# Kernel optimization log

Measured on AMD Instinct MI355X. Metric: run time of the kernel, lower is better.

Reference implementation:

```python
import jax, jax.numpy as jnp
import numpy as np

# Skeleton structure (start, end) connections
REAL_CONNECTIONS = [(0,1),(1,2),(2,3),(3,4),(1,5),(5,6),(6,7),(7,8),(8,9),(8,13),(8,17),(8,21),(8,25),(9,10),(10,11),(11,12),(13,14),(14,15),(15,16),(17,18),(18,19),(19,20),(21,22),(22,23),(23,24),(25,26),(26,27),(27,28),(4,29),(29,30),(29,34),(29,38),(29,42),(29,46),(30,31),(31,32),(32,33),(34,35),(35,36),(36,37),(38,39),(39,40),(40,41),(42,43),(43,44),(44,45),(46,47),(47,48),(48,49)]

def _bone_ranges():
    # dict insertion order matters only for iteration; result is a sum so order-free
    ranges = {(0,1):(0.05,0.15),(1,2):(0.1,0.2),(1,5):(0.1,0.2),(2,3):(0.2,0.35),(3,4):(0.2,0.35),(5,6):(0.2,0.35),(6,7):(0.2,0.35),(4,8):(0.05,0.15),(7,29):(0.05,0.15)}
    for s, e in REAL_CONNECTIONS:
        if 8 <= s < 50 and 8 <= e < 50:
            ranges[(s, e)] = (0.01, 0.08)
    return ranges

_BR = _bone_ranges()
BONE_S = np.array([k[0] for k in _BR], np.int32)
BONE_E = np.array([k[1] for k in _BR], np.int32)
BONE_MIN = np.array([v[0] for v in _BR.values()], np.float32)
BONE_MAX = np.array([v[1] for v in _BR.values()], np.float32)

SYM_L = np.array([8 + i for i in range(21)] + [2, 3, 4], np.int32)
SYM_R = np.array([29 + i for i in range(21)] + [5, 6, 7], np.int32)

ANG_A = np.array([1, 1, 2, 5], np.int32)
ANG_B = np.array([2, 5, 3, 6], np.int32)
ANG_C = np.array([3, 6, 4, 7], np.int32)

CONN_S = np.array([c[0] for c in REAL_CONNECTIONS], np.int32)
CONN_E = np.array([c[1] for c in REAL_CONNECTIONS], np.int32)

DEG = np.float32(180.0 / np.pi)
EPS = np.float32(1e-12)

def _relu(x):
    return jnp.maximum(x, 0.0)

def _normalize(v):
    n = jnp.linalg.norm(v, axis=-1, keepdims=True)
    return v / jnp.maximum(n, EPS)

def setup_inputs() -> dict:
    key = jax.random.key(0)
    k1, k2 = jax.random.split(key)
    B, S, D = 64, 2048, 150
    pred_poses = jax.random.normal(k1, (B, S, D), dtype=jnp.float32)
    target_poses = jax.random.normal(k2, (B, S, D), dtype=jnp.float32)
    return {"pred_poses": pred_poses, "target_poses": target_poses}

def reference(pred_poses, target_poses):
    B, S, _ = pred_poses.shape
    J = pred_poses.reshape(B, S, 50, 3)
    T = target_poses.reshape(B, S, 50, 3)

    # ---- bone length loss (49 constrained bones, one gathered pass) ----
    bv = J[:, :, BONE_E] - J[:, :, BONE_S]                 # [B,S,49,3]
    bl = jnp.linalg.norm(bv, axis=-1)                      # [B,S,49]
    bone_pen = _relu(bl - BONE_MAX) + _relu(BONE_MIN - bl)
    bone_loss = bone_pen.mean()  # == sum over bones of per-bone mean / n_bones

    # ---- joint angle loss (4 triples) ----
    v1 = _normalize(J[:, :, ANG_A] - J[:, :, ANG_B])       # [B,S,4,3]
    v2 = _normalize(J[:, :, ANG_C] - J[:, :, ANG_B])
    cos = jnp.clip(jnp.sum(v1 * v2, axis=-1), -1.0, 1.0)
    deg = jnp.arccos(cos) * DEG
    angle_loss = (_relu(30.0 - deg) + _relu(deg - 150.0)).mean()

    # ---- symmetry loss (24 pairs) ----
    L = J[:, :, SYM_L]                                     # [B,S,24,3]
    R = J[:, :, SYM_R]
    x_sym = jnp.abs(L[..., 0] + R[..., 0])                 # [B,S,24]
    yz_sim = jnp.abs(L[..., 1:] - R[..., 1:]).mean(axis=-1)
    symmetry_loss = (x_sym + yz_sim).mean()

    # ---- temporal consistency ----
    vel = J[:, 1:] - J[:, :-1]                             # [B,S-1,50,3]
    acc = vel[:, 1:] - vel[:, :-1]
    temporal_loss = jnp.linalg.norm(acc, axis=-1).mean() + 0.5 * jnp.linalg.norm(vel, axis=-1).mean()

    # ---- supervised bone-length consistency (all 49 connections) ----
    tb = jnp.linalg.norm(T[:, :, CONN_E] - T[:, :, CONN_S], axis=-1)
    pb = jnp.linalg.norm(J[:, :, CONN_E] - J[:, :, CONN_S], axis=-1)
    supervised_loss = jnp.abs(pb - tb).mean()

    total = (1.0 * bone_loss + 0.5 * angle_loss + 0.3 * symmetry_loss
             + 0.2 * temporal_loss + supervised_loss)
    return bone_loss, angle_loss, symmetry_loss, temporal_loss, supervised_loss, total
```

## Files before the change

kernel.cpp:

```cpp
#include <hip/hip_runtime.h>
#include <math.h>

#define TPB 512
#define CH  32
#define CPB 8

static constexpr int B_     = 64;
static constexpr int S_     = 2048;
static constexpr int TOTAL  = B_ * S_;
static constexpr int NCHUNK = TOTAL / CH;
static constexpr int NBLK   = NCHUNK / CPB;
static constexpr int SAMPB  = 600;
static constexpr int PREDB  = (CH + 2) * SAMPB;
static constexpr int TGTB   = CH * SAMPB;
static constexpr int CHB    = PREDB + TGTB;
static constexpr int NSLICE = 39;
static constexpr int BUFB   = NSLICE * 1024;
static constexpr long TOTB  = (long)TOTAL * SAMPB;

__constant__ int US_[51] = {0,1,1,2,3,5,6,4,7,7,4,
    8,8,8,8,8,9,10,11,13,14,
    15,17,18,19,21,22,23,25,26,27,
    29,29,29,29,29,30,31,32,34,35,
    36,38,39,40,42,43,44,46,47,48};
__constant__ int UE_[51] = {1,2,5,3,4,6,7,8,29,8,29,
    9,13,17,21,25,10,11,12,14,15,
    16,18,19,20,22,23,24,26,27,28,
    30,34,38,42,46,31,32,33,35,36,
    37,39,40,41,43,44,45,47,48,49};
__constant__ float UMIN11_[11] = {0.05f,0.1f,0.1f,0.2f,0.2f,0.2f,0.2f,0.05f,0.05f,-1e9f,-1e9f};
__constant__ float UMAX11_[11] = {0.15f,0.2f,0.2f,0.35f,0.35f,0.35f,0.35f,0.15f,0.15f,1e9f,1e9f};
__constant__ float WSUP11_[11] = {1.f,1.f,1.f,1.f,1.f,1.f,1.f,0.f,0.f,1.f,1.f};
__constant__ int SL_[24] = {8,9,10,11,12,13,14,15,16,17,18,19,20,21,22,23,24,25,26,27,28,2,3,4};
__constant__ int SR_[24] = {29,30,31,32,33,34,35,36,37,38,39,40,41,42,43,44,45,46,47,48,49,5,6,7};
__constant__ int AJ_[4] = {1,1,2,5};
__constant__ int BJ_[4] = {2,5,3,6};
__constant__ int CJ_[4] = {3,6,4,7};

struct F3 { float x, y, z; };
__device__ __forceinline__ F3 ld3(const float* p) { return *(const F3*)p; }
#define SQRTF __builtin_amdgcn_sqrtf

typedef const __attribute__((address_space(1))) void* gas_t;
typedef __attribute__((address_space(3))) void* las_t;

__global__ __launch_bounds__(TPB, 4) void pose_main(
    const float* __restrict__ pred, const float* __restrict__ tgt,
    float* __restrict__ part)
{
    __shared__ __align__(16) char LDS[2 * BUFB];

    const int tid = threadIdx.x;
    const int blk = blockIdx.x;
    const int li  = tid & 15;
    const int g   = tid >> 4;

    const int   uOs0 = US_[g] * 3, uOe0 = UE_[g] * 3;
    const float uMn0 = (g < 11) ? UMIN11_[g] : 0.01f;
    const float uMx0 = (g < 11) ? UMAX11_[g] : 0.08f;
    const float uW0  = (g < 11) ? WSUP11_[g] : 1.f;
    const bool  u1_on = (g < 19);
    const int   k1   = u1_on ? g + 32 : 50;
    const int   uOs1 = US_[k1] * 3, uOe1 = UE_[k1] * 3;
    const bool sy_on = (g < 24);
    const int  ksy = sy_on ? g : 0;
    const int  syL = SL_[ksy] * 3, syR = SR_[ksy] * 3;
    const int aAo = AJ_[g & 3] * 3, aBo = BJ_[g & 3] * 3, aCo = CJ_[g & 3] * 3;
    const int  tO0 = g * 3;
    const int  tO1 = (g + 32) * 3;
    const bool t1_on = (g < 18);

    float a_bone = 0.f, a_ang = 0.f, a_sym = 0.f, a_vel = 0.f, a_acc = 0.f, a_sup = 0.f;

    const int w      = tid >> 6;
    const int lane16 = (tid & 63) << 4;
    auto stage = [&](int cidx, char* lbuf) {
        const long nb = (long)cidx * TGTB;
        const char* pb = (const char*)pred + nb;
        const char* tb = (const char*)tgt  + nb - PREDB;
        const long prem = TOTB - nb - 16;
        #pragma unroll
        for (int s = 0; s < 5; ++s) {
            const int slice = w + s * 8;
            if (slice < NSLICE) {
                const long o = (long)slice * 1024 + lane16;
                const char* src = (o < PREDB)
                    ? pb + (o > prem ? prem : o)
                    : tb + (o > (long)(CHB - 16) ? (long)(CHB - 16) : o);
                __builtin_amdgcn_global_load_lds((gas_t)src, (las_t)(lbuf + slice * 1024), 16, 0, 0);
            }
        }
    };

    const int c0 = blk * CPB;
    stage(c0, LDS);

    #pragma unroll
    for (int c = 0; c < CPB; ++c) {
        char* curb = LDS + (c & 1) * BUFB;
        char* nxtb = LDS + ((c & 1) ^ 1) * BUFB;
        if (c + 1 < CPB) {
            stage(c0 + c + 1, nxtb);
            if (w < 7) asm volatile("s_waitcnt vmcnt(5)" ::: "memory");
            else       asm volatile("s_waitcnt vmcnt(4)" ::: "memory");
        } else {
            asm volatile("s_waitcnt vmcnt(0)" ::: "memory");
        }
        __builtin_amdgcn_s_barrier();
        __builtin_amdgcn_sched_barrier(0);

        const float* Jl = (const float*)curb;
        const float* Tl = Jl + PREDB / 4;
        const int s_base = ((c0 + c) * CH) & (S_ - 1);

        #pragma unroll
        for (int h = 0; h < 2; ++h) {
            const int sb = (li + h * 16) * 150;
            const float* Jp = Jl + sb;
            const float* Tp = Tl + sb;

            auto edge = [&](int so, int eo, float mn, float mx, float wsup) {
                const F3 je = ld3(Jp + eo), js = ld3(Jp + so);
                const float dx = je.x - js.x, dy = je.y - js.y, dz = je.z - js.z;
                const float pb = SQRTF(dx * dx + dy * dy + dz * dz);
                a_bone += fmaxf(pb - mx, 0.f) + fmaxf(mn - pb, 0.f);
                const F3 te = ld3(Tp + eo), ts = ld3(Tp + so);
                const float tx = te.x - ts.x, ty = te.y - ts.y, tz = te.z - ts.z;
                const float tb = SQRTF(tx * tx + ty * ty + tz * tz);
                a_sup += wsup * fabsf(pb - tb);
            };
            edge(uOs0, uOe0, uMn0, uMx0, uW0);
            if (u1_on) edge(uOs1, uOe1, 0.01f, 0.08f, 1.f);

            if (sy_on) {
                const F3 L = ld3(Jp + syL), R = ld3(Jp + syR);
                a_sym += fabsf(L.x + R.x) + 0.5f * (fabsf(L.y - R.y) + fabsf(L.z - R.z));
            }

            if (g < 4) {
                const F3 A = ld3(Jp + aAo), Bb = ld3(Jp + aBo), C = ld3(Jp + aCo);
                const float v1x = A.x - Bb.x, v1y = A.y - Bb.y, v1z = A.z - Bb.z;
                const float v2x = C.x - Bb.x, v2y = C.y - Bb.y, v2z = C.z - Bb.z;
                const float n12 = (v1x*v1x + v1y*v1y + v1z*v1z) * (v2x*v2x + v2y*v2y + v2z*v2z);
                const float inv = __frsqrt_rn(fmaxf(n12, 1e-24f));
                float cosv = (v1x*v2x + v1y*v2y + v1z*v2z) * inv;
                cosv = fminf(fmaxf(cosv, -1.f), 1.f);
                const float deg = acosf(cosv) * 57.29577951308232f;
                a_ang += fmaxf(30.f - deg, 0.f) + fmaxf(deg - 150.f, 0.f);
            }

            {
                const int sidx = s_base + li + h * 16;
                const bool v_ok = sidx < S_ - 1;
                const bool a_ok = sidx < S_ - 2;
                auto temporal = [&](int off) {
                    const F3 p0 = ld3(Jp + off), p1 = ld3(Jp + off + 150), p2 = ld3(Jp + off + 300);
                    if (v_ok) {
                        const float vx = p1.x - p0.x, vy = p1.y - p0.y, vz = p1.z - p0.z;
                        a_vel += SQRTF(vx*vx + vy*vy + vz*vz);
                        if (a_ok) {
                            const float ax = p2.x - 2.f*p1.x + p0.x;
                            const float ay = p2.y - 2.f*p1.y + p0.y;
                            const float az = p2.z - 2.f*p1.z + p0.z;
                            a_acc += SQRTF(ax*ax + ay*ay + az*az);
                        }
                    }
                };
                temporal(tO0);
                if (t1_on) temporal(tO1);
            }
        }

        asm volatile("" ::: "memory");
        __builtin_amdgcn_s_barrier();
    }

    float vals[6] = {a_bone, a_ang, a_sym, a_vel, a_acc, a_sup};
    #pragma unroll
    for (int k = 0; k < 6; ++k)
        #pragma unroll
        for (int off = 32; off > 0; off >>= 1)
            vals[k] += __shfl_down(vals[k], off, 64);

    float* red = (float*)LDS;
    const int lane = tid & 63;
    if (lane == 0) {
        #pragma unroll
        for (int k = 0; k < 6; ++k) red[w * 6 + k] = vals[k];
    }
    __syncthreads();
    if (tid == 0) {
        #pragma unroll
        for (int k = 0; k < 6; ++k) {
            float s = 0.f;
            #pragma unroll
            for (int v = 0; v < 8; ++v) s += red[v * 6 + k];
            part[k * NBLK + blk] = s;
        }
    }
}

__global__ __launch_bounds__(256) void pose_reduce(
    const float* __restrict__ part, float* __restrict__ out)
{
    __shared__ float red[4][6];
    const int tid = threadIdx.x;
    float a[6];
    #pragma unroll
    for (int k = 0; k < 6; ++k) {
        float s = 0.f;
        for (int i = tid; i < NBLK; i += 256) s += part[k * NBLK + i];
        a[k] = s;
    }
    #pragma unroll
    for (int k = 0; k < 6; ++k)
        #pragma unroll
        for (int off = 32; off > 0; off >>= 1)
            a[k] += __shfl_down(a[k], off, 64);

    const int wid = tid >> 6, lane = tid & 63;
    if (lane == 0) {
        #pragma unroll
        for (int k = 0; k < 6; ++k) red[wid][k] = a[k];
    }
    __syncthreads();
    if (tid == 0) {
        float t[6];
        #pragma unroll
        for (int k = 0; k < 6; ++k) t[k] = red[0][k] + red[1][k] + red[2][k] + red[3][k];
        const float bone = t[0] * (1.f / ((float)TOTAL * 49.f));
        const float ang  = t[1] * (1.f / ((float)TOTAL * 4.f));
        const float sym  = t[2] * (1.f / ((float)TOTAL * 24.f));
        const float temporal = t[4] * (1.f / ((float)B_ * (float)(S_ - 2) * 50.f))
                             + 0.5f * t[3] * (1.f / ((float)B_ * (float)(S_ - 1) * 50.f));
        const float sup  = t[5] * (1.f / ((float)TOTAL * 49.f));
        out[0] = bone;
        out[1] = ang;
        out[2] = sym;
        out[3] = temporal;
        out[4] = sup;
        out[5] = bone + 0.5f * ang + 0.3f * sym + 0.2f * temporal + sup;
    }
}

extern "C" void kernel_launch(void* const* d_in, const int* in_sizes, int n_in,
                              void* d_out, int out_size, void* d_ws, size_t ws_size,
                              hipStream_t stream)
{
    const float* pred = (const float*)d_in[0];
    const float* tgt  = (const float*)d_in[1];
    float* part = (float*)d_ws;
    pose_main<<<NBLK, TPB, 0, stream>>>(pred, tgt, part);
    pose_reduce<<<1, 256, 0, stream>>>(part, (float*)d_out);
}
```

Before: 39.64 us.

## Fuse final reduction into main kernel and regroup bone and temporal work

```diff
diff --git a/kernel.cpp b/kernel.cpp
--- a/kernel.cpp
+++ b/kernel.cpp
@@ -18,19 +18,9 @@
 static constexpr int BUFB   = NSLICE * 1024;
 static constexpr long TOTB  = (long)TOTAL * SAMPB;
 
-__constant__ int US_[51] = {0,1,1,2,3,5,6,4,7,7,4,
-    8,8,8,8,8,9,10,11,13,14,
-    15,17,18,19,21,22,23,25,26,27,
-    29,29,29,29,29,30,31,32,34,35,
-    36,38,39,40,42,43,44,46,47,48};
-__constant__ int UE_[51] = {1,2,5,3,4,6,7,8,29,8,29,
-    9,13,17,21,25,10,11,12,14,15,
-    16,18,19,20,22,23,24,26,27,28,
-    30,34,38,42,46,31,32,33,35,36,
-    37,39,40,41,43,44,45,47,48,49};
-__constant__ float UMIN11_[11] = {0.05f,0.1f,0.1f,0.2f,0.2f,0.2f,0.2f,0.05f,0.05f,-1e9f,-1e9f};
-__constant__ float UMAX11_[11] = {0.15f,0.2f,0.2f,0.35f,0.35f,0.35f,0.35f,0.15f,0.15f,1e9f,1e9f};
-__constant__ float WSUP11_[11] = {1.f,1.f,1.f,1.f,1.f,1.f,1.f,0.f,0.f,1.f,1.f};
+__constant__ int CA_[26] = {0,2,1,6,7,  8,10,8,14,8,18,8,22,8,26,  29,31,29,35,29,39,29,43,29,47, 4};
+__constant__ int CB_[26] = {1,3,5,7,29, 9,11,13,15,17,19,21,23,25,27, 30,32,34,36,38,40,42,44,46,48, 8};
+__constant__ int CC_[26] = {2,4,6,8,4,  10,12,14,16,18,20,22,24,26,28, 31,33,35,37,39,41,43,45,47,49, 8};
 __constant__ int SL_[24] = {8,9,10,11,12,13,14,15,16,17,18,19,20,21,22,23,24,25,26,27,28,2,3,4};
 __constant__ int SR_[24] = {29,30,31,32,33,34,35,36,37,38,39,40,41,42,43,44,45,46,47,48,49,5,6,7};
 __constant__ int AJ_[4] = {1,1,2,5};
@@ -46,29 +36,35 @@
 
 __global__ __launch_bounds__(TPB, 4) void pose_main(
     const float* __restrict__ pred, const float* __restrict__ tgt,
-    float* __restrict__ part)
+    float* __restrict__ part, int* __restrict__ cnt, float* __restrict__ out)
 {
     __shared__ __align__(16) char LDS[2 * BUFB];
+    __shared__ int lastflag;
 
     const int tid = threadIdx.x;
     const int blk = blockIdx.x;
     const int li  = tid & 15;
     const int g   = tid >> 4;
 
-    const int   uOs0 = US_[g] * 3, uOe0 = UE_[g] * 3;
-    const float uMn0 = (g < 11) ? UMIN11_[g] : 0.01f;
-    const float uMx0 = (g < 11) ? UMAX11_[g] : 0.08f;
-    const float uW0  = (g < 11) ? WSUP11_[g] : 1.f;
-    const bool  u1_on = (g < 19);
-    const int   k1   = u1_on ? g + 32 : 50;
-    const int   uOs1 = US_[k1] * 3, uOe1 = UE_[k1] * 3;
+    const int gg  = (g < 26) ? g : 0;
+    const int cAo = CA_[gg] * 3, cBo = CB_[gg] * 3, cCo = CC_[gg] * 3;
+    float mn1 = 0.01f, mx1 = 0.08f, w1 = 1.f;
+    float mn2 = 0.01f, mx2 = 0.08f, w2 = 1.f;
+    if      (g == 0)  { mn1=0.05f; mx1=0.15f;        mn2=0.1f;  mx2=0.2f;  }
+    else if (g == 1)  { mn1=0.2f;  mx1=0.35f;        mn2=0.2f;  mx2=0.35f; }
+    else if (g == 2)  { mn1=0.1f;  mx1=0.2f;         mn2=0.2f;  mx2=0.35f; }
+    else if (g == 3)  { mn1=0.2f;  mx1=0.35f;        mn2=-1e9f; mx2=1e9f;  }
+    else if (g == 4)  { mn1=0.05f; mx1=0.15f; w1=0.f; mn2=-1e9f; mx2=1e9f; }
+    else if (g == 25) { mn1=0.05f; mx1=0.15f; w1=0.f; mn2=-1e9f; mx2=1e9f; w2=0.f; }
     const bool sy_on = (g < 24);
     const int  ksy = sy_on ? g : 0;
     const int  syL = SL_[ksy] * 3, syR = SR_[ksy] * 3;
-    const int aAo = AJ_[g & 3] * 3, aBo = BJ_[g & 3] * 3, aCo = CJ_[g & 3] * 3;
-    const int  tO0 = g * 3;
-    const int  tO1 = (g + 32) * 3;
-    const bool t1_on = (g < 18);
+    const int aAo = AJ_[g & 3] * 3, aBo = BJ_[g & 3] * 3, aCo2 = CJ_[g & 3] * 3;
+    const bool tp_on = (tid < 400);
+    const int  jq  = tid % 50;
+    const int  rq  = tid / 50;
+    const int  tbase = (rq * 4) * 150 + jq * 3;
+    const int  ss  = rq * 4;
 
     float a_bone = 0.f, a_ang = 0.f, a_sym = 0.f, a_vel = 0.f, a_acc = 0.f, a_sup = 0.f;
 
@@ -95,7 +91,7 @@
     const int c0 = blk * CPB;
     stage(c0, LDS);
 
-    #pragma unroll
+    #pragma unroll 2
     for (int c = 0; c < CPB; ++c) {
         char* curb = LDS + (c & 1) * BUFB;
         char* nxtb = LDS + ((c & 1) ^ 1) * BUFB;
@@ -119,18 +115,21 @@
             const float* Jp = Jl + sb;
             const float* Tp = Tl + sb;
 
-            auto edge = [&](int so, int eo, float mn, float mx, float wsup) {
-                const F3 je = ld3(Jp + eo), js = ld3(Jp + so);
-                const float dx = je.x - js.x, dy = je.y - js.y, dz = je.z - js.z;
-                const float pb = SQRTF(dx * dx + dy * dy + dz * dz);
-                a_bone += fmaxf(pb - mx, 0.f) + fmaxf(mn - pb, 0.f);
-                const F3 te = ld3(Tp + eo), ts = ld3(Tp + so);
-                const float tx = te.x - ts.x, ty = te.y - ts.y, tz = te.z - ts.z;
-                const float tb = SQRTF(tx * tx + ty * ty + tz * tz);
-                a_sup += wsup * fabsf(pb - tb);
-            };
-            edge(uOs0, uOe0, uMn0, uMx0, uW0);
-            if (u1_on) edge(uOs1, uOe1, 0.01f, 0.08f, 1.f);
+            if (g < 26) {
+                const F3 jA = ld3(Jp + cAo), jB = ld3(Jp + cBo), jC = ld3(Jp + cCo);
+                float dx = jA.x - jB.x, dy = jA.y - jB.y, dz = jA.z - jB.z;
+                const float len1 = SQRTF(dx*dx + dy*dy + dz*dz);
+                dx = jB.x - jC.x; dy = jB.y - jC.y; dz = jB.z - jC.z;
+                const float len2 = SQRTF(dx*dx + dy*dy + dz*dz);
+                a_bone += fmaxf(len1 - mx1, 0.f) + fmaxf(mn1 - len1, 0.f)
+                        + fmaxf(len2 - mx2, 0.f) + fmaxf(mn2 - len2, 0.f);
+                const F3 tA = ld3(Tp + cAo), tB = ld3(Tp + cBo), tC = ld3(Tp + cCo);
+                dx = tA.x - tB.x; dy = tA.y - tB.y; dz = tA.z - tB.z;
+                const float tl1 = SQRTF(dx*dx + dy*dy + dz*dz);
+                dx = tB.x - tC.x; dy = tB.y - tC.y; dz = tB.z - tC.z;
+                const float tl2 = SQRTF(dx*dx + dy*dy + dz*dz);
+                a_sup += w1 * fabsf(len1 - tl1) + w2 * fabsf(len2 - tl2);
+            }
 
             if (sy_on) {
                 const F3 L = ld3(Jp + syL), R = ld3(Jp + syR);
@@ -138,7 +137,7 @@
             }
 
             if (g < 4) {
-                const F3 A = ld3(Jp + aAo), Bb = ld3(Jp + aBo), C = ld3(Jp + aCo);
+                const F3 A = ld3(Jp + aAo), Bb = ld3(Jp + aBo), C = ld3(Jp + aCo2);
                 const float v1x = A.x - Bb.x, v1y = A.y - Bb.y, v1z = A.z - Bb.z;
                 const float v2x = C.x - Bb.x, v2y = C.y - Bb.y, v2z = C.z - Bb.z;
                 const float n12 = (v1x*v1x + v1y*v1y + v1z*v1z) * (v2x*v2x + v2y*v2y + v2z*v2z);
@@ -148,26 +147,31 @@
                 const float deg = acosf(cosv) * 57.29577951308232f;
                 a_ang += fmaxf(30.f - deg, 0.f) + fmaxf(deg - 150.f, 0.f);
             }
-
-            {
-                const int sidx = s_base + li + h * 16;
-                const bool v_ok = sidx < S_ - 1;
-                const bool a_ok = sidx < S_ - 2;
-                auto temporal = [&](int off) {
-                    const F3 p0 = ld3(Jp + off), p1 = ld3(Jp + off + 150), p2 = ld3(Jp + off + 300);
-                    if (v_ok) {
-                        const float vx = p1.x - p0.x, vy = p1.y - p0.y, vz = p1.z - p0.z;
-                        a_vel += SQRTF(vx*vx + vy*vy + vz*vz);
-                        if (a_ok) {
-                            const float ax = p2.x - 2.f*p1.x + p0.x;
-                            const float ay = p2.y - 2.f*p1.y + p0.y;
-                            const float az = p2.z - 2.f*p1.z + p0.z;
-                            a_acc += SQRTF(ax*ax + ay*ay + az*az);
-                        }
+        }
+
+        if (tp_on) {
+            F3 q0 = ld3(Jl + tbase);
+            F3 q1 = ld3(Jl + tbase + 150);
+            F3 q2 = ld3(Jl + tbase + 300);
+            F3 q3 = ld3(Jl + tbase + 450);
+            F3 q4 = ld3(Jl + tbase + 600);
+            F3 q5 = ld3(Jl + tbase + 750);
+            const F3 qs[6] = {q0, q1, q2, q3, q4, q5};
+            #pragma unroll
+            for (int i = 0; i < 4; ++i) {
+                const int sidx = s_base + ss + i;
+                if (sidx < S_ - 1) {
+                    const float vx = qs[i+1].x - qs[i].x;
+                    const float vy = qs[i+1].y - qs[i].y;
+                    const float vz = qs[i+1].z - qs[i].z;
+                    a_vel += SQRTF(vx*vx + vy*vy + vz*vz);
+                    if (sidx < S_ - 2) {
+                        const float ax = qs[i+2].x - 2.f*qs[i+1].x + qs[i].x;
+                        const float ay = qs[i+2].y - 2.f*qs[i+1].y + qs[i].y;
+                        const float az = qs[i+2].z - 2.f*qs[i+1].z + qs[i].z;
+                        a_acc += SQRTF(ax*ax + ay*ay + az*az);
                     }
-                };
-                temporal(tO0);
-                if (t1_on) temporal(tO1);
+                }
             }
         }
 
@@ -198,48 +202,37 @@
             part[k * NBLK + blk] = s;
         }
     }
-}
-
-__global__ __launch_bounds__(256) void pose_reduce(
-    const float* __restrict__ part, float* __restrict__ out)
-{
-    __shared__ float red[4][6];
-    const int tid = threadIdx.x;
-    float a[6];
-    #pragma unroll
-    for (int k = 0; k < 6; ++k) {
+
+    __threadfence();
+    if (tid == 0) lastflag = (atomicAdd(cnt, 1) == NBLK - 1) ? 1 : 0;
+    __syncthreads();
+    if (lastflag) {
+        __threadfence();
+        const int k = tid >> 6;
         float s = 0.f;
-        for (int i = tid; i < NBLK; i += 256) s += part[k * NBLK + i];
-        a[k] = s;
-    }
-    #pragma unroll
-    for (int k = 0; k < 6; ++k)
-        #pragma unroll
-        for (int off = 32; off > 0; off >>= 1)
-            a[k] += __shfl_down(a[k], off, 64);
-
-    const int wid = tid >> 6, lane = tid & 63;
-    if (lane == 0) {
-        #pragma unroll
-        for (int k = 0; k < 6; ++k) red[wid][k] = a[k];
-    }
-    __syncthreads();
-    if (tid == 0) {
-        float t[6];
-        #pragma unroll
-        for (int k = 0; k < 6; ++k) t[k] = red[0][k] + red[1][k] + red[2][k] + red[3][k];
-        const float bone = t[0] * (1.f / ((float)TOTAL * 49.f));
-        const float ang  = t[1] * (1.f / ((float)TOTAL * 4.f));
-        const float sym  = t[2] * (1.f / ((float)TOTAL * 24.f));
-        const float temporal = t[4] * (1.f / ((float)B_ * (float)(S_ - 2) * 50.f))
-                             + 0.5f * t[3] * (1.f / ((float)B_ * (float)(S_ - 1) * 50.f));
-        const float sup  = t[5] * (1.f / ((float)TOTAL * 49.f));
-        out[0] = bone;
-        out[1] = ang;
-        out[2] = sym;
-        out[3] = temporal;
-        out[4] = sup;
-        out[5] = bone + 0.5f * ang + 0.3f * sym + 0.2f * temporal + sup;
+        if (k < 6) {
+            volatile const float* vp = part + k * NBLK;
+            #pragma unroll
+            for (int m = 0; m < NBLK; m += 64) s += vp[m + lane];
+            #pragma unroll
+            for (int off = 32; off > 0; off >>= 1) s += __shfl_down(s, off, 64);
+            if (lane == 0) red[64 + k] = s;
+        }
+        __syncthreads();
+        if (tid == 0) {
+            const float bone = red[64] * (1.f / ((float)TOTAL * 49.f));
+            const float ang  = red[65] * (1.f / ((float)TOTAL * 4.f));
+            const float sym  = red[66] * (1.f / ((float)TOTAL * 24.f));
+            const float temporal = red[68] * (1.f / ((float)B_ * (float)(S_ - 2) * 50.f))
+                                 + 0.5f * red[67] * (1.f / ((float)B_ * (float)(S_ - 1) * 50.f));
+            const float sup  = red[69] * (1.f / ((float)TOTAL * 49.f));
+            out[0] = bone;
+            out[1] = ang;
+            out[2] = sym;
+            out[3] = temporal;
+            out[4] = sup;
+            out[5] = bone + 0.5f * ang + 0.3f * sym + 0.2f * temporal + sup;
+        }
     }
 }
 
@@ -250,6 +243,7 @@
     const float* pred = (const float*)d_in[0];
     const float* tgt  = (const float*)d_in[1];
     float* part = (float*)d_ws;
-    pose_main<<<NBLK, TPB, 0, stream>>>(pred, tgt, part);
-    pose_reduce<<<1, 256, 0, stream>>>(part, (float*)d_out);
+    int*   cnt  = (int*)((char*)d_ws + 6 * NBLK * 4);
+    hipMemsetAsync(cnt, 0, 4, stream);
+    pose_main<<<NBLK, TPB, 0, stream>>>(pred, tgt, part, cnt, (float*)d_out);
 }
```

New measurement: 112.2 us. 183% more time.
